# Kernel tuning notes

Measured on AMD Instinct MI355X. Metric: run time of the kernel, lower is better.

## Reference

```python
import jax, jax.numpy as jnp
import numpy as np

B, T_PREV, T_CUR = 256, 128, 129
N_COV, N_TREAT, N_CONF = 30, 57, 5
H, FC = 128, 128
D_IN = N_COV + N_TREAT            # 87, lstm external input size
D_CELL = D_IN + N_CONF            # 92, cell input = [x_t, z_{t-1}]


def setup_inputs() -> dict:
    key = jax.random.key(0)
    ks = jax.random.split(key, 18)
    s = 0.05
    return {
        "previous_covariates": jax.random.normal(ks[0], (B, T_PREV, N_COV), jnp.float32),
        "previous_treatments": jax.random.normal(ks[1], (B, T_PREV, N_TREAT), jnp.float32),
        "current_covariates": jax.random.normal(ks[2], (B, T_CUR, N_COV), jnp.float32),
        "init_input": jax.random.normal(ks[3], (1, 1, D_IN), jnp.float32) * s,
        "h0": jax.random.normal(ks[4], (1, H), jnp.float32) * s,
        "c0": jax.random.normal(ks[5], (1, H), jnp.float32) * s,
        "z0": jax.random.normal(ks[6], (1, N_CONF), jnp.float32) * s,
        "W_ih": jax.random.normal(ks[7], (4 * H, D_CELL), jnp.float32) * s,
        "W_hh": jax.random.normal(ks[8], (4 * H, H), jnp.float32) * s,
        "b_ih": jax.random.normal(ks[9], (4 * H,), jnp.float32) * s,
        "b_hh": jax.random.normal(ks[10], (4 * H,), jnp.float32) * s,
        "W_z": jax.random.normal(ks[11], (N_CONF, H), jnp.float32) * s,
        "b_z": jax.random.normal(ks[12], (N_CONF,), jnp.float32) * s,
        "dec_W1": jax.random.normal(ks[13], (N_TREAT, N_COV + N_CONF, FC), jnp.float32) * s,
        "dec_b1": jax.random.normal(ks[14], (N_TREAT, FC), jnp.float32) * s,
        "dec_W2": jax.random.normal(ks[15], (N_TREAT, FC), jnp.float32) * s,
        "dec_b2": jax.random.normal(ks[16], (N_TREAT,), jnp.float32) * s,
    }


def _forward(previous_covariates, previous_treatments, current_covariates,
             init_input, h0, c0, z0, W_ih, W_hh, b_ih, b_hh, W_z, b_z,
             dec_W1, dec_b1, dec_W2, dec_b2):
    Bn = previous_covariates.shape[0]
    # (T_PREV, B, D_IN)
    x = jnp.concatenate([previous_covariates, previous_treatments], -1).transpose(1, 0, 2)
    # prepend trainable init input -> (T_CUR, B, D_IN)
    rnn_in = jnp.concatenate([jnp.broadcast_to(init_input, (1, Bn, D_IN)), x], 0)

    bias = b_ih + b_hh

    def step(carry, xt):
        h, c, z = carry
        inp = jnp.concatenate([xt, z], -1)                 # (B, D_CELL)
        gates = inp @ W_ih.T + h @ W_hh.T + bias           # (B, 4H)
        i, f, g, o = jnp.split(gates, 4, axis=-1)          # torch LSTMCell gate order
        c = jax.nn.sigmoid(f) * c + jax.nn.sigmoid(i) * jnp.tanh(g)
        h = jax.nn.sigmoid(o) * jnp.tanh(c)
        z = h @ W_z.T + b_z                                # (B, N_CONF)
        return (h, c, z), z

    carry0 = (jnp.broadcast_to(h0, (Bn, H)),
              jnp.broadcast_to(c0, (Bn, H)),
              jnp.broadcast_to(z0, (Bn, N_CONF)))
    _, zs = jax.lax.scan(step, carry0, rnn_in)             # (T_CUR, B, N_CONF)

    hidden_confounders = zs.reshape(-1, N_CONF)            # (T_CUR*B, N_CONF)
    covariates = current_covariates.transpose(1, 0, 2).reshape(-1, N_COV)
    # shapes match by construction (T_CUR*B rows each) -> no pad branch
    multitask_input = jnp.concatenate([hidden_confounders, covariates], -1)  # (N, 35)

    # batched per-treatment Linear -> LeakyReLU(0.01) -> Linear
    hdec = jax.nn.leaky_relu(
        jnp.einsum('nc,tcf->ntf', multitask_input, dec_W1) + dec_b1, 0.01)
    preds = jnp.einsum('ntf,tf->nt', hdec, dec_W2) + dec_b2                   # (N, 57)

    # T_CUR*B % (T_PREV) == 0 with these shapes -> no element trim
    confounders = hidden_confounders.reshape(T_PREV, -1, N_CONF)              # (128, 258, 5)
    return preds, confounders


def reference(previous_covariates, previous_treatments, current_covariates,
              init_input, h0, c0, z0, W_ih, W_hh, b_ih, b_hh, W_z, b_z,
              dec_W1, dec_b1, dec_W2, dec_b2):
    return _forward(previous_covariates, previous_treatments, current_covariates,
                    init_input, h0, c0, z0, W_ih, W_hh, b_ih, b_hh, W_z, b_z,
                    dec_W1, dec_b1, dec_W2, dec_b2)
```

## Files before the change

### kernel.cpp

```cpp
#include <hip/hip_runtime.h>
#include <stdint.h>

#define BATCH 256
#define T_PREVN 128
#define T_CURN 129
#define N_COV 30
#define N_TREAT 57
#define N_CONF 5
#define HID 128
#define D_IN 87
#define D_CELL 92
#define GATES 512
#define PRED_N (T_CURN*BATCH)
#define CONF_OFF (PRED_N*N_TREAT)
#define WS_NEED (57*8*2*64*8*2)

typedef _Float16 h2 __attribute__((ext_vector_type(2)));
typedef _Float16 h8 __attribute__((ext_vector_type(8)));
typedef float f32x4 __attribute__((ext_vector_type(4)));

__device__ inline float rcp_fast(float x){
#if __has_builtin(__builtin_amdgcn_rcpf)
    return __builtin_amdgcn_rcpf(x);
#else
    return 1.0f / x;
#endif
}
__device__ inline float sigmoid_f(float x){ return rcp_fast(1.0f + __expf(-x)); }
__device__ inline float tanh_f(float x){ return 1.0f - 2.0f*rcp_fast(1.0f + __expf(2.0f*x)); }

__device__ inline float dot2f(h2 a, h2 b, float c){
#if __has_builtin(__builtin_amdgcn_fdot2)
    return __builtin_amdgcn_fdot2(a, b, c, false);
#else
    return c + (float)a.x*(float)b.x + (float)a.y*(float)b.y;
#endif
}
__device__ inline unsigned short f2us(float v){
    _Float16 h = (_Float16)v;
    return __builtin_bit_cast(unsigned short, h);
}
__device__ inline h2 us2h2(unsigned int u){
    return __builtin_bit_cast(h2, u);
}

__global__ __launch_bounds__(1024, 4) void lstm_scan(
    const float* __restrict__ pc, const float* __restrict__ pt,
    const float* __restrict__ init_input, const float* __restrict__ h0,
    const float* __restrict__ c0, const float* __restrict__ z0,
    const float* __restrict__ W_ih, const float* __restrict__ W_hh,
    const float* __restrict__ b_ih, const float* __restrict__ b_hh,
    const float* __restrict__ W_z, const float* __restrict__ b_z,
    float* __restrict__ zs_out)
{
    const int b   = blockIdx.x;
    const int tid = threadIdx.x;
    const int g   = tid >> 1;
    const int hf  = tid & 1;

    __shared__ alignas(16) unsigned short v16[224];
    __shared__ alignas(16) unsigned short xall[T_CURN*88];
    __shared__ alignas(16) unsigned short hall[T_CURN*136];
    __shared__ alignas(16) float gbuf[GATES];
    __shared__ alignas(16) _Float16 wz16[5*HID];
    __shared__ float z0c[5];

    float wzg[5];
    #pragma unroll
    for (int z = 0; z < 5; z++) wzg[z] = W_ih[g*D_CELL + 87 + z];

    float be = b_ih[g] + b_hh[g];
    #pragma unroll
    for (int z = 0; z < 5; z++) be += wzg[z] * b_z[z];

    h2 w[56];
    if (hf == 0){
        #pragma unroll
        for (int i = 0; i < 43; i++){
            h2 p; p.x = (_Float16)W_ih[g*D_CELL + 2*i];
                  p.y = (_Float16)W_ih[g*D_CELL + 2*i + 1];
            w[i] = p;
        }
        { h2 p; p.x = (_Float16)W_ih[g*D_CELL + 86]; p.y = (_Float16)0.0f; w[43] = p; }
        #pragma unroll
        for (int i = 44; i < 56; i++){
            const int u = 2*(i - 44);
            float f0 = W_hh[g*HID + u], f1 = W_hh[g*HID + u + 1];
            #pragma unroll
            for (int z = 0; z < 5; z++){
                f0 += wzg[z]*W_z[z*HID + u];
                f1 += wzg[z]*W_z[z*HID + u + 1];
            }
            h2 p; p.x = (_Float16)f0; p.y = (_Float16)f1;
            w[i] = p;
        }
    } else {
        #pragma unroll
        for (int i = 0; i < 52; i++){
            const int u = 24 + 2*i;
            float f0 = W_hh[g*HID + u], f1 = W_hh[g*HID + u + 1];
            #pragma unroll
            for (int z = 0; z < 5; z++){
                f0 += wzg[z]*W_z[z*HID + u];
                f1 += wzg[z]*W_z[z*HID + u + 1];
            }
            h2 p; p.x = (_Float16)f0; p.y = (_Float16)f1;
            w[i] = p;
        }
        #pragma unroll
        for (int i = 52; i < 56; i++){ h2 p; p.x=(_Float16)0.f; p.y=(_Float16)0.f; w[i]=p; }
    }

    for (int idx = tid; idx < T_CURN*88; idx += 1024){
        const int row = idx / 88;
        const int col = idx - row*88;
        float v = 0.0f;
        if (col < D_IN){
            if (row == 0) v = init_input[col];
            else {
                const int tp = row - 1;
                v = (col < N_COV) ? pc[(b*T_PREVN + tp)*N_COV + col]
                                  : pt[(b*T_PREVN + tp)*N_TREAT + (col - N_COV)];
            }
        }
        xall[idx] = f2us(v);
    }

    float c = 0.0f;
    if (tid < HID){ v16[88 + tid] = f2us(h0[tid]); c = c0[tid]; }
    if (tid >= 216 && tid < 224) v16[tid] = 0;

    if (tid < 5){
        float acc0 = 0.0f, acc1 = 0.0f;
        #pragma unroll 8
        for (int u = 0; u < HID; u += 2){
            acc0 += W_z[tid*HID + u]     * h0[u];
            acc1 += W_z[tid*HID + u + 1] * h0[u + 1];
        }
        z0c[tid] = z0[tid] - b_z[tid] - (acc0 + acc1);
    }
    __syncthreads();

    if (tid >= 128 && tid < 216) v16[tid - 128] = xall[tid - 128];
    float b0 = be;
    #pragma unroll
    for (int z = 0; z < 5; z++) b0 += wzg[z] * z0c[z];
    __syncthreads();

    const unsigned short* vbase = v16 + hf*112;
    for (int t = 0; t < T_CURN; t++){
        float a0 = 0.f, a1 = 0.f, a2 = 0.f, a3 = 0.f;
        #pragma unroll
        for (int i = 0; i < 14; i++){
            const uint4 q = *(const uint4*)(vbase + i*8);
            a0 = dot2f(w[4*i+0], us2h2(q.x), a0);
            a1 = dot2f(w[4*i+1], us2h2(q.y), a1);
            a2 = dot2f(w[4*i+2], us2h2(q.z), a2);
            a3 = dot2f(w[4*i+3], us2h2(q.w), a3);
        }
        float s = (a0 + a1) + (a2 + a3);
        s += __shfl_xor(s, 1);
        if (hf == 0) gbuf[g] = s + ((t == 0) ? b0 : be);
        __syncthreads();

        if (tid < HID){
            const float gi = gbuf[tid];
            const float gf = gbuf[128 + tid];
            const float gg = gbuf[256 + tid];
            const float go = gbuf[384 + tid];
            c = sigmoid_f(gf)*c + sigmoid_f(gi)*tanh_f(gg);
            const float h = sigmoid_f(go)*tanh_f(c);
            const unsigned short hu = f2us(h);
            v16[88 + tid] = hu;
            hall[t*136 + tid] = hu;
        } else if (tid < 216){
            if (t < T_PREVN) v16[tid - 128] = xall[(t + 1)*88 + (tid - 128)];
        }
        __syncthreads();
    }

    for (int i = tid; i < 5*HID; i += 1024) wz16[i] = (_Float16)W_z[i];
    __syncthreads();

    if (tid < T_CURN*N_CONF){
        const int t  = tid / 5;
        const int zi = tid - t*5;
        const uint4* hr = (const uint4*)(hall + t*136);
        const uint4* wr = (const uint4*)(wz16 + zi*HID);
        float a0 = 0.f, a1 = 0.f;
        #pragma unroll
        for (int i = 0; i < 16; i++){
            const uint4 hq = hr[i];
            const uint4 wq = wr[i];
            a0 = dot2f(us2h2(hq.x), us2h2(wq.x), a0);
            a1 = dot2f(us2h2(hq.y), us2h2(wq.y), a1);
            a0 = dot2f(us2h2(hq.z), us2h2(wq.z), a0);
            a1 = dot2f(us2h2(hq.w), us2h2(wq.w), a1);
        }
        zs_out[(t*BATCH + b)*N_CONF + zi] = a0 + a1 + b_z[zi];
    }
}

__global__ __launch_bounds__(256) void prepack_w1(const float* __restrict__ dW1,
                                                  _Float16* __restrict__ wsh)
{
    const int tid = blockIdx.x*256 + threadIdx.x;
    const int treat = tid >> 10;
    const int r     = tid & 1023;
    const int ft    = r >> 7;
    const int ks    = (r >> 6) & 1;
    const int l     = r & 63;
    const int col   = ft*16 + (l & 15);
    const int kb    = ks*32 + ((l >> 4) << 3);
    h8 v;
    #pragma unroll
    for (int j = 0; j < 8; j++){
        const int k = kb + j;
        v[j] = (k < 35) ? (_Float16)dW1[(treat*35 + k)*128 + col] : (_Float16)0.0f;
    }
    *(h8*)(wsh + (size_t)tid*8) = v;
}

__global__ __launch_bounds__(256) void decoder_mfma(
    const float* __restrict__ cc, const float* __restrict__ zs,
    const _Float16* __restrict__ wsh,
    const float* __restrict__ db1, const float* __restrict__ dW2,
    const float* __restrict__ db2, float* __restrict__ preds)
{
    __shared__ alignas(16) _Float16 m_lds[64*72];

    const int tid  = threadIdx.x;
    const int base = blockIdx.x * 64;
    const int t    = base >> 8;

    for (int idx = tid; idx < 64*72; idx += 256){
        const int r = idx / 72;
        const int j = idx - r*72;
        const int n = base + r;
        const int b = n & 255;
        float v = 0.0f;
        if (j < 5)       v = zs[n*N_CONF + j];
        else if (j < 35) v = cc[(b*T_CURN + t)*N_COV + (j - 5)];
        m_lds[r*72 + j] = (_Float16)v;
    }
    __syncthreads();

    const int w    = tid >> 6;
    const int l    = tid & 63;
    const int row  = l & 15;
    const int quad = l >> 4;

    const _Float16* arow = m_lds + (w*16 + row)*72 + quad*8;
    const h8 a0 = *(const h8*)(arow);
    const h8 a1 = *(const h8*)(arow + 32);
    const int nbase = base + w*16 + quad*4;

    for (int treat = 0; treat < 57; treat++){
        const _Float16* bp = wsh + (size_t)treat*8192 + l*8;
        f32x4 pred = {0.0f, 0.0f, 0.0f, 0.0f};
        #pragma unroll
        for (int ft = 0; ft < 8; ft++){
            const h8 b0 = *(const h8*)(bp + ft*1024);
            const h8 b1 = *(const h8*)(bp + ft*1024 + 512);
            f32x4 acc = {0.0f, 0.0f, 0.0f, 0.0f};
            acc = __builtin_amdgcn_mfma_f32_16x16x32_f16(a0, b0, acc, 0, 0, 0);
            acc = __builtin_amdgcn_mfma_f32_16x16x32_f16(a1, b1, acc, 0, 0, 0);
            const int col = ft*16 + row;
            const float hb1 = db1[treat*128 + col];
            const float hw2 = dW2[treat*128 + col];
            #pragma unroll
            for (int r = 0; r < 4; r++){
                float hd = acc[r] + hb1;
                hd = (hd > 0.0f) ? hd : 0.01f*hd;
                pred[r] += hd * hw2;
            }
        }
        #pragma unroll
        for (int r = 0; r < 4; r++){
            float s = pred[r];
            s += __shfl_xor(s, 1);
            s += __shfl_xor(s, 2);
            s += __shfl_xor(s, 4);
            s += __shfl_xor(s, 8);
            pred[r] = s;
        }
        if (row == 0){
            const float b2 = db2[treat];
            #pragma unroll
            for (int r = 0; r < 4; r++)
                preds[(size_t)(nbase + r)*N_TREAT + treat] = pred[r] + b2;
        }
    }
}

__global__ __launch_bounds__(256) void decoder_fallback(
    const float* __restrict__ cc, const float* __restrict__ zs,
    const float* __restrict__ dW1, const float* __restrict__ db1,
    const float* __restrict__ dW2, const float* __restrict__ db2,
    float* __restrict__ preds)
{
    const int t     = blockIdx.x;
    const int treat = blockIdx.y;
    const int tid   = threadIdx.x;

    __shared__ alignas(16) float w1t[128*36];
    __shared__ float b1s[128];
    __shared__ float w2s[128];

    for (int it = tid; it < 35*128; it += 256){
        const int cidx = it >> 7;
        const int f    = it & 127;
        w1t[f*36 + cidx] = dW1[(treat*35 + cidx)*128 + f];
    }
    if (tid < 128){
        b1s[tid] = db1[treat*128 + tid];
        w2s[tid] = dW2[treat*128 + tid];
        w1t[tid*36 + 35] = 0.0f;
    }
    __syncthreads();

    const int n = t*BATCH + tid;
    float m[36];
    #pragma unroll
    for (int j = 0; j < N_CONF; j++) m[j] = zs[n*N_CONF + j];
    #pragma unroll
    for (int j = 0; j < N_COV; j++)  m[N_CONF + j] = cc[(tid*T_CURN + t)*N_COV + j];
    m[35] = 0.0f;

    const float b2 = db2[treat];
    float pred = 0.0f;
    for (int f = 0; f < 128; f++){
        float a = b1s[f];
        const float4* wr = (const float4*)(w1t + f*36);
        #pragma unroll
        for (int cq = 0; cq < 9; cq++){
            const float4 v = wr[cq];
            a += m[cq*4+0]*v.x + m[cq*4+1]*v.y + m[cq*4+2]*v.z + m[cq*4+3]*v.w;
        }
        a = (a > 0.0f) ? a : 0.01f*a;
        pred += a * w2s[f];
    }
    preds[n*N_TREAT + treat] = pred + b2;
}

extern "C" void kernel_launch(void* const* d_in, const int* in_sizes, int n_in,
                              void* d_out, int out_size, void* d_ws, size_t ws_size,
                              hipStream_t stream)
{
    const float* pc   = (const float*)d_in[0];
    const float* pt   = (const float*)d_in[1];
    const float* cc   = (const float*)d_in[2];
    const float* init = (const float*)d_in[3];
    const float* h0   = (const float*)d_in[4];
    const float* c0   = (const float*)d_in[5];
    const float* z0   = (const float*)d_in[6];
    const float* W_ih = (const float*)d_in[7];
    const float* W_hh = (const float*)d_in[8];
    const float* b_ih = (const float*)d_in[9];
    const float* b_hh = (const float*)d_in[10];
    const float* W_z  = (const float*)d_in[11];
    const float* b_z  = (const float*)d_in[12];
    const float* dW1  = (const float*)d_in[13];
    const float* db1  = (const float*)d_in[14];
    const float* dW2  = (const float*)d_in[15];
    const float* db2  = (const float*)d_in[16];

    float* preds = (float*)d_out;
    float* zs    = (float*)d_out + CONF_OFF;

    const bool use_mfma = (ws_size >= (size_t)WS_NEED);

    if (use_mfma)
        prepack_w1<<<228, 256, 0, stream>>>(dW1, (_Float16*)d_ws);

    lstm_scan<<<BATCH, 1024, 0, stream>>>(pc, pt, init, h0, c0, z0,
                                          W_ih, W_hh, b_ih, b_hh, W_z, b_z, zs);

    if (use_mfma)
        decoder_mfma<<<516, 256, 0, stream>>>(cc, zs, (const _Float16*)d_ws,
                                              db1, dW2, db2, preds);
    else
        decoder_fallback<<<dim3(T_CURN, N_TREAT), 256, 0, stream>>>(
            cc, zs, dW1, db1, dW2, db2, preds);
}
```

Measured before the change: 256.2 us.

## Restructure decoder per treatment with register-resident weights and packed fp16 input matrix

Adds a pre-pass that writes covariates into a packed fp16 multitask matrix in workspace, and has the LSTM write its confounders into the same matrix. A new decoder grid runs one block per (treatment, row-group): it keeps that treatment's W1 MFMA fragments, biases and W2 in registers and streams row tiles through MFMA, so weights are not reloaded for every row block. The cost is an extra kernel launch, extra workspace traffic, and stores to preds strided by treatment. If the workspace is too small, the older decoder path is used.

Measured after the change: 224.3 us. -12.5%, faster.

```diff
diff --git a/kernel.cpp b/kernel.cpp
--- a/kernel.cpp
+++ b/kernel.cpp
@@ -14,8 +14,11 @@
 #define PRED_N (T_CURN*BATCH)
 #define CONF_OFF (PRED_N*N_TREAT)
 #define WS_NEED (57*8*2*64*8*2)
+#define MT_ELEMS (PRED_N*40)
+#define WS_NEED2 (WS_NEED + MT_ELEMS*2)
 
 typedef _Float16 h2 __attribute__((ext_vector_type(2)));
+typedef _Float16 h4 __attribute__((ext_vector_type(4)));
 typedef _Float16 h8 __attribute__((ext_vector_type(8)));
 typedef float f32x4 __attribute__((ext_vector_type(4)));
 
@@ -51,7 +54,7 @@
     const float* __restrict__ W_ih, const float* __restrict__ W_hh,
     const float* __restrict__ b_ih, const float* __restrict__ b_hh,
     const float* __restrict__ W_z, const float* __restrict__ b_z,
-    float* __restrict__ zs_out)
+    float* __restrict__ zs_out, _Float16* __restrict__ mT)
 {
     const int b   = blockIdx.x;
     const int tid = threadIdx.x;
@@ -197,7 +200,10 @@
             a0 = dot2f(us2h2(hq.z), us2h2(wq.z), a0);
             a1 = dot2f(us2h2(hq.w), us2h2(wq.w), a1);
         }
-        zs_out[(t*BATCH + b)*N_CONF + zi] = a0 + a1 + b_z[zi];
+        const float z = a0 + a1 + b_z[zi];
+        const int n = t*BATCH + b;
+        zs_out[(size_t)n*N_CONF + zi] = z;
+        if (mT) mT[(size_t)n*40 + zi] = (_Float16)z;
     }
 }
 
@@ -219,6 +225,92 @@
         v[j] = (k < 35) ? (_Float16)dW1[(treat*35 + k)*128 + col] : (_Float16)0.0f;
     }
     *(h8*)(wsh + (size_t)tid*8) = v;
+}
+
+__global__ __launch_bounds__(256) void mt_cov(const float* __restrict__ cc,
+                                              _Float16* __restrict__ mT)
+{
+    const int tid = blockIdx.x*256 + threadIdx.x;
+    const int n = tid / 40;
+    const int c = tid - n*40;
+    if (c < 5) return;
+    float v = 0.0f;
+    if (c < 35){
+        const int b = n & 255;
+        const int t = n >> 8;
+        v = cc[(b*T_CURN + t)*N_COV + (c - 5)];
+    }
+    mT[tid] = (_Float16)v;
+}
+
+__global__ __launch_bounds__(256, 2) void decoder_treat(
+    const _Float16* __restrict__ mT, const _Float16* __restrict__ wsh,
+    const float* __restrict__ db1, const float* __restrict__ dW2,
+    const float* __restrict__ db2, float* __restrict__ preds)
+{
+    const int treat = blockIdx.x;
+    const int rg    = blockIdx.y;
+    const int w     = threadIdx.x >> 6;
+    const int l     = threadIdx.x & 63;
+    const int q     = l >> 4;
+    const int r16   = l & 15;
+
+    h8 bf0[8], bf1[8];
+    const _Float16* bp = wsh + (size_t)treat*8192 + l*8;
+    #pragma unroll
+    for (int ft = 0; ft < 8; ft++){
+        bf0[ft] = *(const h8*)(bp + ft*1024);
+        bf1[ft] = *(const h8*)(bp + ft*1024 + 512);
+    }
+    float b1r[8], w2r[8], w2c[8];
+    #pragma unroll
+    for (int ft = 0; ft < 8; ft++){
+        b1r[ft] = db1[treat*128 + ft*16 + r16];
+        w2r[ft] = dW2[treat*128 + ft*16 + r16];
+        w2c[ft] = 0.01f * w2r[ft];
+    }
+    const float b2 = db2[treat];
+
+    const int tend = (rg + 1)*258;
+    for (int tile = rg*258 + w; tile < tend; tile += 4){
+        const int n = tile*16 + r16;
+        const _Float16* mrow = mT + (size_t)n*40;
+        const h8 a0 = *(const h8*)(mrow + q*8);
+        h8 a1 = {};
+        if (q == 0){
+            const h4 t4 = *(const h4*)(mrow + 32);
+            a1[0] = t4[0]; a1[1] = t4[1]; a1[2] = t4[2]; a1[3] = t4[3];
+        }
+
+        f32x4 pred = {0.f, 0.f, 0.f, 0.f};
+        #pragma unroll
+        for (int ft = 0; ft < 8; ft++){
+            f32x4 acc = {b1r[ft], b1r[ft], b1r[ft], b1r[ft]};
+            acc = __builtin_amdgcn_mfma_f32_16x16x32_f16(a0, bf0[ft], acc, 0, 0, 0);
+            acc = __builtin_amdgcn_mfma_f32_16x16x32_f16(a1, bf1[ft], acc, 0, 0, 0);
+            #pragma unroll
+            for (int r = 0; r < 4; r++){
+                const float a  = acc[r];
+                const float mx = fmaxf(a, 0.0f);
+                const float mn = fminf(a, 0.0f);
+                pred[r] += mx*w2r[ft] + mn*w2c[ft];
+            }
+        }
+        #pragma unroll
+        for (int r = 0; r < 4; r++){
+            float s = pred[r];
+            s += __shfl_xor(s, 1);
+            s += __shfl_xor(s, 2);
+            s += __shfl_xor(s, 4);
+            s += __shfl_xor(s, 8);
+            pred[r] = s;
+        }
+        if (r16 == 0){
+            #pragma unroll
+            for (int r = 0; r < 4; r++)
+                preds[(size_t)(tile*16 + q*4 + r)*N_TREAT + treat] = pred[r] + b2;
+        }
+    }
 }
 
 __global__ __launch_bounds__(256) void decoder_mfma(
@@ -368,17 +460,25 @@
     float* preds = (float*)d_out;
     float* zs    = (float*)d_out + CONF_OFF;
 
-    const bool use_mfma = (ws_size >= (size_t)WS_NEED);
-
-    if (use_mfma)
-        prepack_w1<<<228, 256, 0, stream>>>(dW1, (_Float16*)d_ws);
+    const bool ws_full = (ws_size >= (size_t)WS_NEED2);
+    const bool ws_w1   = (ws_size >= (size_t)WS_NEED);
+
+    _Float16* wsh = (_Float16*)d_ws;
+    _Float16* mT  = (_Float16*)((char*)d_ws + WS_NEED);
+
+    if (ws_w1)
+        prepack_w1<<<228, 256, 0, stream>>>(dW1, wsh);
+    if (ws_full)
+        mt_cov<<<5160, 256, 0, stream>>>(cc, mT);
 
     lstm_scan<<<BATCH, 1024, 0, stream>>>(pc, pt, init, h0, c0, z0,
-                                          W_ih, W_hh, b_ih, b_hh, W_z, b_z, zs);
-
-    if (use_mfma)
-        decoder_mfma<<<516, 256, 0, stream>>>(cc, zs, (const _Float16*)d_ws,
-                                              db1, dW2, db2, preds);
+                                          W_ih, W_hh, b_ih, b_hh, W_z, b_z,
+                                          zs, ws_full ? mT : (_Float16*)nullptr);
+
+    if (ws_full)
+        decoder_treat<<<dim3(N_TREAT, 8), 256, 0, stream>>>(mT, wsh, db1, dW2, db2, preds);
+    else if (ws_w1)
+        decoder_mfma<<<516, 256, 0, stream>>>(cc, zs, wsh, db1, dW2, db2, preds);
     else
         decoder_fallback<<<dim3(T_CURN, N_TREAT), 256, 0, stream>>>(
             cc, zs, dW1, db1, dW2, db2, preds);
```
